# Kernel optimization log

Hardware: AMD Instinct MI355X
Metric: run time of the kernel (lower is better)

Reference implementation:

```python
import jax, jax.numpy as jnp
import numpy as np

L = 11
THETA_DIV = 5
OMEGA0 = 6
BLUR_K = 7
BLUR_SIGMA = 4.0


def _make_psi(j_scale):
    # Morlet wavelet bank exactly as np.fromfunction in the torch module
    c = L // 2
    k = np.arange(THETA_DIV, dtype=np.float64)[:, None, None]
    i = np.arange(L, dtype=np.float64)[None, :, None]
    jj = np.arange(L, dtype=np.float64)[None, None, :]
    scale = 2.0 * 2.0 ** (2 * j_scale)
    arg = (1j * OMEGA0 * ((i - c) * np.cos(np.pi * k / THETA_DIV)
                          - (jj - c) * np.sin(np.pi * k / THETA_DIV)) / scale
           - ((i - c) ** 2 + (jj - c) ** 2) / scale)
    return (1.0 / (np.sqrt(2.0 * np.pi) * 2.0 ** j_scale)) * np.exp(arg)


def _make_blur_kernel():
    # 7x7 Gaussian, sigma=4, normalized to sum 1 (standard GaussianBlur)
    c = (BLUR_K - 1) / 2.0
    x = np.arange(BLUR_K, dtype=np.float64) - c
    g = np.exp(-(x ** 2) / (2.0 * BLUR_SIGMA ** 2))
    k2 = np.outer(g, g)
    return (k2 / k2.sum()).astype(np.float32)


def setup_inputs() -> dict:
    key = jax.random.key(0)
    img = jax.random.normal(key, (8, 1, 256, 256), dtype=jnp.float32)
    psi = np.concatenate([_make_psi(3), _make_psi(0)], axis=0)  # [10,11,11] complex
    psi_re = jnp.asarray(psi.real.astype(np.float32)[:, None, :, :])  # [10,1,11,11]
    psi_im = jnp.asarray(psi.imag.astype(np.float32)[:, None, :, :])
    blur_k = jnp.asarray(_make_blur_kernel())  # [7,7]
    return {"img": img, "psi_re": psi_re, "psi_im": psi_im, "blur_k": blur_k}


def _conv(x, w, groups=1, pad=5):
    return jax.lax.conv_general_dilated(
        x, w, window_strides=(1, 1), padding=[(pad, pad), (pad, pad)],
        dimension_numbers=("NCHW", "OIHW", "NCHW"), feature_group_count=groups)


def _blur(x, blur_k):
    # depthwise Gaussian blur, padding 'same'
    C = x.shape[1]
    w = jnp.tile(blur_k[None, None], (C, 1, 1, 1))  # [C,1,7,7]
    return _conv(x, w, groups=C, pad=BLUR_K // 2)


def reference(img, psi_re, psi_im, blur_k):
    # s0: blurred input, strided downsample by 8
    s0 = _blur(img, blur_k)[:, :, ::8, ::8]

    # s1 = conv2d(img_complex, psi1): img is real, so split into re/im real convs
    s1_re = _conv(img, psi_re)            # [N,10,H,W]
    s1_im = _conv(img, psi_im)
    s1_abs = jnp.sqrt(s1_re * s1_re + s1_im * s1_im)
    # blurred s1 is later cast to double -> only its real part survives;
    # blur is a real-linear op so Re(blur(s1)) = blur(Re(s1))
    s1_out = _blur(s1_re, blur_k)[:, :, ::8, ::8]

    # s2 = grouped conv of |s1| with psi2 (psi1 tiled over 10 groups)
    psi2_re = jnp.tile(psi_re, (10, 1, 1, 1))  # [100,1,11,11]
    # only real part of blur(s2) reaches the output (cast to double)
    s2_re = _conv(s1_abs, psi2_re, groups=10)  # [N,100,H,W]
    s2_out = _blur(s2_re, blur_k)[:, :, ::8, ::8]

    feature = jnp.concatenate([s0, s1_out, s2_out], axis=1)  # [N,111,H/8,W/8]
    N = feature.shape[0]
    return feature.reshape(N, -1)
```

## Files before the change

kernel.cpp:

```cpp
#include <hip/hip_runtime.h>
#include <math.h>


#define PIMG_SZ (288 * 288)
#define FHP_OFF (8 * PIMG_SZ)
#define SSTR  284
#define W1    298
#define S1SZ  (17 * 298)
#define IVSTR 300
#define IVPL  (17 * 300)
#define CSTR  600

__global__ __launch_bounds__(256) void k_prep(const float* __restrict__ img,
                                              const float* __restrict__ psi_re,
                                              const float* __restrict__ psi_im,
                                              const float* __restrict__ blur,
                                              float* __restrict__ pimg,
                                              float* __restrict__ fhp) {
    int bid = blockIdx.x, tid = threadIdx.x;
    if (bid < 288) {
        int n = bid / 36, rg = bid - n * 36;
        float* dst = pimg + n * PIMG_SZ + rg * 8 * 288;
        const float* src = img + n * 65536;
        for (int i = tid; i < 576; i += 256) {
            int lr = i / 72, c4 = i - lr * 72;
            int prow = rg * 8 + lr;
            int irow = prow - 16;
            float4 v = {0.f, 0.f, 0.f, 0.f};
            if (irow >= 0 && irow < 256 && c4 >= 4 && c4 < 68)
                v = *(const float4*)(src + irow * 256 + 4 * c4 - 16);
            *(float4*)(dst + lr * 288 + 4 * c4) = v;
        }
        return;
    }
    for (int g = tid; g < 1360; g += 256) {
        int ch = g / 136;
        int w = g - ch * 136;
        int part = w / 17;
        int i = w - part * 17;
        const float* pr = psi_re + ch * 121;
        const float* pi = psi_im + ch * 121;
        float val = 0.f;
        if (part < 4) {
            int qmin = (part >= 2) ? 3 : 0;
            int comp = part & 1;
            float bden = blur[24];
            for (int q = qmin; q < 7; ++q) {
                int jj = i - q;
                if (jj < 0 || jj > 10) continue;
                float bq = blur[21 + q] / bden;
                float hh = comp ? pi[55 + jj] : pr[55 + jj];
                val += bq * hh;
            }
        } else {
            int pmin = (part >= 6) ? 3 : 0;
            int comp = part & 1;
            float dr = pr[60], di = pi[60];
            float inv = 1.f / (dr * dr + di * di);
            for (int p = pmin; p < 7; ++p) {
                int ii = i - p;
                if (ii < 0 || ii > 10) continue;
                float ap = blur[p * 7 + 3];
                float nr = pr[ii * 11 + 5], ni = pi[ii * 11 + 5];
                float f = comp ? (ni * dr - nr * di) * inv
                               : (nr * dr + ni * di) * inv;
                val += ap * f;
            }
        }
        fhp[g] = val;
    }
}

__global__ __launch_bounds__(512, 4) void k_fused4(const float* __restrict__ pimg,
                                                   const float* __restrict__ psi_re,
                                                   const float* __restrict__ psi_im,
                                                   const float* __restrict__ blur,
                                                   const float* __restrict__ fhp,
                                                   float* __restrict__ out) {
    __shared__ __align__(16) float bufA[10132];
    __shared__ __align__(16) float bufB[10200];
    const int tid = threadIdx.x;
    const int lane = tid & 63;
    const int wave = tid >> 6;
    const int Y = blockIdx.x;
    const int src2 = blockIdx.y;
    const int n = blockIdx.z;
    size_t nb = (size_t)n * 111 * 1024;

    const bool isimg = (src2 == 0);
    const bool paired = (src2 >= 3);
    int ga = 0, gb = 0;
    if (src2 == 1) ga = gb = 0;
    else if (src2 == 2) ga = gb = 5;
    else if (paired) {
        int p2 = src2 - 3;
        ga = (p2 < 2) ? 1 + p2 : 4 + p2;
        gb = (p2 < 2) ? 4 - p2 : 11 - p2;
    }

    if (isimg) {
        const float* gp = pimg + n * PIMG_SZ + (8 * Y + 8) * 288 + 8;
        for (int idx = tid; idx < 17 * 68; idx += 512) {
            int r = idx / 68, c4 = idx - r * 68;
            float4 v = *(const float4*)(gp + r * 288 + 4 * c4);
            int c = 4 * c4;
            int d = r * W1 + c + (c >> 3);
            bufA[d] = v.x; bufA[d + 1] = v.y; bufA[d + 2] = v.z; bufA[d + 3] = v.w;
        }
    } else {
        const float* pr = psi_re + ga * 121;
        const float* pi = psi_im + ga * 121;
        float dr = pr[60], di = pi[60];
        float inv = rsqrtf(dr * dr + di * di);

        const float* gp = pimg + n * PIMG_SZ + (8 * Y + 3) * 288 + 8;
        for (int idx = tid; idx < 27 * 68; idx += 512) {
            int r = idx / 68, c4 = idx - r * 68;
            *(float4*)(bufA + r * SSTR + 4 * c4) = *(const float4*)(gp + r * 288 + 4 * c4);
        }
        __syncthreads();

        for (int task = tid; task < 532; task += 512) {
            int rg = (task >= 266) ? 1 : 0;
            int v = task - rg * 266;
            int r0 = rg * 8;
            const float* sp = bufA + r0 * SSTR + v + 3;
            float xv[18];
#pragma unroll
            for (int p = 0; p < 18; ++p) xv[p] = sp[p * SSTR];
            int dsw = v + (v >> 3);
            float* dR = bufB + r0 * IVSTR + dsw;
#pragma unroll
            for (int m = 0; m < 8; ++m) {
                float ar = 0.f, ai = 0.f;
#pragma unroll
                for (int p = 0; p < 11; ++p) {
                    ar = fmaf(pr[p * 11 + 5], xv[m + p], ar);
                    ai = fmaf(pi[p * 11 + 5], xv[m + p], ai);
                }
                dR[m * IVSTR] = ar;
                dR[m * IVSTR + IVPL] = ai;
            }
        }
        if (tid < 266) {
            int v = tid;
            const float* sp = bufA + 16 * SSTR + v + 3;
            float ar = 0.f, ai = 0.f;
#pragma unroll
            for (int p = 0; p < 11; ++p) {
                float x = sp[p * SSTR];
                ar = fmaf(pr[p * 11 + 5], x, ar);
                ai = fmaf(pi[p * 11 + 5], x, ai);
            }
            int dsw = v + (v >> 3);
            bufB[16 * IVSTR + dsw] = ar;
            bufB[16 * IVSTR + IVPL + dsw] = ai;
        }
        __syncthreads();

        int rowbase = 8 * Y - 8;
        for (int t2 = tid; t2 < 544; t2 += 512) {
            int r = t2 >> 5, xg = t2 & 31;
            int ry = rowbase + r;
            int wb = r * W1 + 9 * xg + 9;
            if (ry >= 0 && ry < 256) {
                const float* sR = bufB + r * IVSTR + 9 * xg;
                float xr[18], xi[18];
#pragma unroll
                for (int j = 0; j < 18; ++j) {
                    int off = j + (j >> 3);
                    xr[j] = sR[off];
                    xi[j] = sR[off + IVPL];
                }
                if (paired) {
#pragma unroll
                    for (int m = 0; m < 8; ++m) {
                        float a = 0.f, b = 0.f, c = 0.f, d = 0.f;
#pragma unroll
                        for (int j = 0; j < 11; ++j) {
                            float hr = pr[55 + j], hi2 = pi[55 + j];
                            a = fmaf(hr, xr[m + j], a);
                            b = fmaf(hi2, xi[m + j], b);
                            c = fmaf(hr, xi[m + j], c);
                            d = fmaf(hi2, xr[m + j], d);
                        }
                        float e1 = a - b, o1 = c + d;
                        float e2 = a + b, o2 = c - d;
                        bufA[wb + m]        = inv * sqrtf(fmaf(e1, e1, o1 * o1));
                        bufA[S1SZ + wb + m] = inv * sqrtf(fmaf(e2, e2, o2 * o2));
                    }
                } else {
#pragma unroll
                    for (int m = 0; m < 8; ++m) {
                        float sr = 0.f, si = 0.f;
#pragma unroll
                        for (int j = 0; j < 11; ++j) {
                            float hr = pr[55 + j], hi2 = pi[55 + j];
                            sr = fmaf(hr, xr[m + j], fmaf(-hi2, xi[m + j], sr));
                            si = fmaf(hr, xi[m + j], fmaf(hi2, xr[m + j], si));
                        }
                        bufA[wb + m] = inv * sqrtf(fmaf(sr, sr, si * si));
                    }
                }
            } else {
#pragma unroll
                for (int m = 0; m < 8; ++m) {
                    bufA[wb + m] = 0.f;
                    if (paired) bufA[S1SZ + wb + m] = 0.f;
                }
            }
        }
        if (tid < 17) {
            int r = tid;
#pragma unroll
            for (int t = 0; t < 8; ++t) {
                bufA[r * W1 + t] = 0.f;
                if (paired) bufA[S1SZ + r * W1 + t] = 0.f;
            }
            bufA[r * W1 + 297] = 0.f;
            if (paired) bufA[S1SZ + r * W1 + 297] = 0.f;
        }
    }
    __syncthreads();

    {
        int kh = __builtin_amdgcn_readfirstlane(wave >> 2);
        int fro = (Y == 0) ? 102 : 68;
        int fio = (Y == 0) ? 119 : 85;
        const float* s1base = bufA + (paired ? kh * S1SZ : 0);
        auto doC = [&](int t) {
            int tsw = t + (t >> 3);
            float v[17];
#pragma unroll
            for (int i = 0; i < 17; ++i) v[i] = s1base[i * W1 + tsw];
            int nk = paired ? 6 : 3;
            for (int kk = 0; kk < nk; ++kk) {
                int k, p;
                if (paired) { k = (kk < 3) ? kk : kk + 2; p = kh * 6 + kk; }
                else        { k = kh * 5 + kk;            p = kh * 3 + kk; }
                const float* fR = fhp + k * 136 + fro;
                const float* fI = fhp + k * 136 + fio;
                float cr = 0.f, ci = 0.f;
#pragma unroll
                for (int i = 0; i < 17; ++i) {
                    cr = fmaf(fR[i], v[i], cr);
                    ci = fmaf(fI[i], v[i], ci);
                }
                bufB[p * CSTR + tsw] = cr;
                bufB[p * CSTR + 300 + tsw] = ci;
            }
        };
        doC(((wave & 3) << 6) + lane);
        if (lane < 9 && (wave == 0 || wave == 4))
            doC(256 + lane);
    }
    __syncthreads();

    int nout = paired ? 384 : 192;
    if (tid < nout) {
        int chsel = paired ? (tid >= 192) : 0;
        int t3 = tid - chsel * 192;
        int s = t3 >> 5, X = t3 & 31;
        int kdist = (s < 3) ? s : s + 2;
        int p = chsel * 6 + s;
        const float* hb = fhp + kdist * 136 + ((X == 0) ? 34 : 0);
        const float* cR = bufB + p * CSTR + 9 * X;
        float u = 0.f, v2 = 0.f;
#pragma unroll
        for (int j = 0; j < 17; ++j) {
            int off = j + (j >> 3);
            u  = fmaf(hb[j], cR[off], u);
            v2 = fmaf(hb[17 + j], cR[off + 300], v2);
        }
        int g = chsel ? gb : ga;
        int ch0 = isimg ? 1 : 11 + g * 10;
        out[nb + (size_t)(ch0 + kdist) * 1024 + Y * 32 + X] = u - v2;
        if (s == 1 || s == 2 || s == 4 || s == 5) {
            int partner = (s < 3) ? 5 - s : 13 - s;
            out[nb + (size_t)(ch0 + partner) * 1024 + Y * 32 + X] = u + v2;
        }
    } else if (isimg && tid < 224) {
        int X = tid - 192;
        float s0 = 0.f;
#pragma unroll
        for (int p = 0; p < 7; ++p)
#pragma unroll
            for (int q = 0; q < 7; ++q) {
                int c = 8 * X + q + 5;
                s0 = fmaf(blur[p * 7 + q], bufA[(p + 5) * W1 + c + (c >> 3)], s0);
            }
        out[nb + Y * 32 + X] = s0;
    }
}

extern "C" void kernel_launch(void* const* d_in, const int* in_sizes, int n_in,
                              void* d_out, int out_size, void* d_ws, size_t ws_size,
                              hipStream_t stream) {
    const float* img    = (const float*)d_in[0];
    const float* psi_re = (const float*)d_in[1];
    const float* psi_im = (const float*)d_in[2];
    const float* blur   = (const float*)d_in[3];
    float* out = (float*)d_out;
    float* ws = (float*)d_ws;
    float* pimg = ws;
    float* fhp  = ws + FHP_OFF;

    k_prep<<<289, 256, 0, stream>>>(img, psi_re, psi_im, blur, pimg, fhp);

    dim3 g2(32, 7, 8);
    k_fused4<<<g2, 512, 0, stream>>>(pimg, psi_re, psi_im, blur, fhp, out);
}
```

Baseline: 61.26 us.

## Split fused kernel into image and paired-group kernels with unrolled accumulators

The single multi-role kernel is split into two kernels. A dedicated image kernel handles the input-blur and first-order outputs with a smaller shared-memory footprint. A specialized paired kernel treats every wavelet group, including the two self-paired groups 0 and 5, through the paired path, so the role branches disappear. The column-filter stage is rewritten to read each shared value once and update six (or three) real/imag accumulator pairs in a fully unrolled loop. In exchange, the self-paired groups now do duplicate paired work and write their outputs from both halves, and there is an extra kernel launch.

```diff
diff --git a/kernel.cpp b/kernel.cpp
--- a/kernel.cpp
+++ b/kernel.cpp
@@ -71,155 +71,201 @@
     }
 }
 
-__global__ __launch_bounds__(512, 4) void k_fused4(const float* __restrict__ pimg,
-                                                   const float* __restrict__ psi_re,
-                                                   const float* __restrict__ psi_im,
-                                                   const float* __restrict__ blur,
-                                                   const float* __restrict__ fhp,
-                                                   float* __restrict__ out) {
+__global__ __launch_bounds__(512, 2) void k_img(const float* __restrict__ pimg,
+                                                const float* __restrict__ blur,
+                                                const float* __restrict__ fhp,
+                                                float* __restrict__ out) {
+    __shared__ __align__(16) float bufA[5080];
+    __shared__ __align__(16) float bufB[3600];
+    const int tid = threadIdx.x;
+    const int lane = tid & 63;
+    const int wave = tid >> 6;
+    const int Y = blockIdx.x;
+    const int n = blockIdx.z;
+    size_t nb = (size_t)n * 111 * 1024;
+
+    const float* gp = pimg + n * PIMG_SZ + (8 * Y + 8) * 288 + 8;
+    for (int idx = tid; idx < 17 * 68; idx += 512) {
+        int r = idx / 68, c4 = idx - r * 68;
+        float4 v = *(const float4*)(gp + r * 288 + 4 * c4);
+        int c = 4 * c4;
+        int d = r * W1 + c + (c >> 3);
+        bufA[d] = v.x; bufA[d + 1] = v.y; bufA[d + 2] = v.z; bufA[d + 3] = v.w;
+    }
+    __syncthreads();
+
+    {
+        int kh = __builtin_amdgcn_readfirstlane(wave >> 2);
+        int fro = (Y == 0) ? 102 : 68;
+        int fio = (Y == 0) ? 119 : 85;
+        const float* fb = fhp + kh * 680;
+        auto doC = [&](int t) {
+            int tsw = t + (t >> 3);
+            float cr0 = 0.f, ci0 = 0.f, cr1 = 0.f, ci1 = 0.f, cr2 = 0.f, ci2 = 0.f;
+#pragma unroll
+            for (int i = 0; i < 17; ++i) {
+                float v = bufA[i * W1 + tsw];
+                cr0 = fmaf(fb[fro + i], v, cr0);        ci0 = fmaf(fb[fio + i], v, ci0);
+                cr1 = fmaf(fb[136 + fro + i], v, cr1);  ci1 = fmaf(fb[136 + fio + i], v, ci1);
+                cr2 = fmaf(fb[272 + fro + i], v, cr2);  ci2 = fmaf(fb[272 + fio + i], v, ci2);
+            }
+            int p = kh * 3;
+            bufB[p * CSTR + tsw] = cr0;       bufB[p * CSTR + 300 + tsw] = ci0;
+            bufB[(p + 1) * CSTR + tsw] = cr1; bufB[(p + 1) * CSTR + 300 + tsw] = ci1;
+            bufB[(p + 2) * CSTR + tsw] = cr2; bufB[(p + 2) * CSTR + 300 + tsw] = ci2;
+        };
+        doC(((wave & 3) << 6) + lane);
+        if (lane < 9 && (wave == 0 || wave == 4)) doC(256 + lane);
+    }
+    __syncthreads();
+
+    if (tid < 192) {
+        int s = tid >> 5, X = tid & 31;
+        int kdist = (s < 3) ? s : s + 2;
+        const float* hb = fhp + kdist * 136 + ((X == 0) ? 34 : 0);
+        const float* cR = bufB + s * CSTR + 9 * X;
+        float u = 0.f, v2 = 0.f;
+#pragma unroll
+        for (int j = 0; j < 17; ++j) {
+            int off = j + (j >> 3);
+            u  = fmaf(hb[j], cR[off], u);
+            v2 = fmaf(hb[17 + j], cR[off + 300], v2);
+        }
+        out[nb + (size_t)(1 + kdist) * 1024 + Y * 32 + X] = u - v2;
+        if (s == 1 || s == 2 || s == 4 || s == 5) {
+            int partner = (s < 3) ? 5 - s : 13 - s;
+            out[nb + (size_t)(1 + partner) * 1024 + Y * 32 + X] = u + v2;
+        }
+    } else if (tid < 224) {
+        int X = tid - 192;
+        float s0 = 0.f;
+#pragma unroll
+        for (int p = 0; p < 7; ++p)
+#pragma unroll
+            for (int q = 0; q < 7; ++q) {
+                int c = 8 * X + q + 5;
+                s0 = fmaf(blur[p * 7 + q], bufA[(p + 5) * W1 + c + (c >> 3)], s0);
+            }
+        out[nb + Y * 32 + X] = s0;
+    }
+}
+
+__global__ __launch_bounds__(512, 4) void k_pairk(const float* __restrict__ pimg,
+                                                  const float* __restrict__ psi_re,
+                                                  const float* __restrict__ psi_im,
+                                                  const float* __restrict__ fhp,
+                                                  float* __restrict__ out) {
     __shared__ __align__(16) float bufA[10132];
     __shared__ __align__(16) float bufB[10200];
     const int tid = threadIdx.x;
     const int lane = tid & 63;
     const int wave = tid >> 6;
     const int Y = blockIdx.x;
-    const int src2 = blockIdx.y;
+    const int pidx = blockIdx.y;
     const int n = blockIdx.z;
     size_t nb = (size_t)n * 111 * 1024;
 
-    const bool isimg = (src2 == 0);
-    const bool paired = (src2 >= 3);
-    int ga = 0, gb = 0;
-    if (src2 == 1) ga = gb = 0;
-    else if (src2 == 2) ga = gb = 5;
-    else if (paired) {
-        int p2 = src2 - 3;
-        ga = (p2 < 2) ? 1 + p2 : 4 + p2;
-        gb = (p2 < 2) ? 4 - p2 : 11 - p2;
-    }
-
-    if (isimg) {
-        const float* gp = pimg + n * PIMG_SZ + (8 * Y + 8) * 288 + 8;
-        for (int idx = tid; idx < 17 * 68; idx += 512) {
-            int r = idx / 68, c4 = idx - r * 68;
-            float4 v = *(const float4*)(gp + r * 288 + 4 * c4);
-            int c = 4 * c4;
-            int d = r * W1 + c + (c >> 3);
-            bufA[d] = v.x; bufA[d + 1] = v.y; bufA[d + 2] = v.z; bufA[d + 3] = v.w;
-        }
-    } else {
-        const float* pr = psi_re + ga * 121;
-        const float* pi = psi_im + ga * 121;
-        float dr = pr[60], di = pi[60];
-        float inv = rsqrtf(dr * dr + di * di);
-
-        const float* gp = pimg + n * PIMG_SZ + (8 * Y + 3) * 288 + 8;
-        for (int idx = tid; idx < 27 * 68; idx += 512) {
-            int r = idx / 68, c4 = idx - r * 68;
-            *(float4*)(bufA + r * SSTR + 4 * c4) = *(const float4*)(gp + r * 288 + 4 * c4);
-        }
-        __syncthreads();
-
-        for (int task = tid; task < 532; task += 512) {
-            int rg = (task >= 266) ? 1 : 0;
-            int v = task - rg * 266;
-            int r0 = rg * 8;
-            const float* sp = bufA + r0 * SSTR + v + 3;
-            float xv[18];
-#pragma unroll
-            for (int p = 0; p < 18; ++p) xv[p] = sp[p * SSTR];
-            int dsw = v + (v >> 3);
-            float* dR = bufB + r0 * IVSTR + dsw;
+    const int gtab_a[6] = {0, 5, 1, 2, 6, 7};
+    const int gtab_b[6] = {0, 5, 4, 3, 9, 8};
+    int ga = gtab_a[pidx], gb = gtab_b[pidx];
+
+    const float* pr = psi_re + ga * 121;
+    const float* pi = psi_im + ga * 121;
+    float dr = pr[60], di = pi[60];
+    float inv = rsqrtf(dr * dr + di * di);
+
+    const float* gp = pimg + n * PIMG_SZ + (8 * Y + 3) * 288 + 8;
+    for (int idx = tid; idx < 27 * 68; idx += 512) {
+        int r = idx / 68, c4 = idx - r * 68;
+        *(float4*)(bufA + r * SSTR + 4 * c4) = *(const float4*)(gp + r * 288 + 4 * c4);
+    }
+    __syncthreads();
+
+    for (int task = tid; task < 532; task += 512) {
+        int rg = (task >= 266) ? 1 : 0;
+        int v = task - rg * 266;
+        int r0 = rg * 8;
+        const float* sp = bufA + r0 * SSTR + v + 3;
+        float xv[18];
+#pragma unroll
+        for (int p = 0; p < 18; ++p) xv[p] = sp[p * SSTR];
+        int dsw = v + (v >> 3);
+        float* dR = bufB + r0 * IVSTR + dsw;
+#pragma unroll
+        for (int m = 0; m < 8; ++m) {
+            float ar = 0.f, ai = 0.f;
+#pragma unroll
+            for (int p = 0; p < 11; ++p) {
+                ar = fmaf(pr[p * 11 + 5], xv[m + p], ar);
+                ai = fmaf(pi[p * 11 + 5], xv[m + p], ai);
+            }
+            dR[m * IVSTR] = ar;
+            dR[m * IVSTR + IVPL] = ai;
+        }
+    }
+    if (tid < 266) {
+        int v = tid;
+        const float* sp = bufA + 16 * SSTR + v + 3;
+        float ar = 0.f, ai = 0.f;
+#pragma unroll
+        for (int p = 0; p < 11; ++p) {
+            float x = sp[p * SSTR];
+            ar = fmaf(pr[p * 11 + 5], x, ar);
+            ai = fmaf(pi[p * 11 + 5], x, ai);
+        }
+        int dsw = v + (v >> 3);
+        bufB[16 * IVSTR + dsw] = ar;
+        bufB[16 * IVSTR + IVPL + dsw] = ai;
+    }
+    __syncthreads();
+
+    int rowbase = 8 * Y - 8;
+    for (int t2 = tid; t2 < 544; t2 += 512) {
+        int r = t2 >> 5, xg = t2 & 31;
+        int ry = rowbase + r;
+        int wb = r * W1 + 9 * xg + 9;
+        if (ry >= 0 && ry < 256) {
+            const float* sR = bufB + r * IVSTR + 9 * xg;
+            float xr[18], xi[18];
+#pragma unroll
+            for (int j = 0; j < 18; ++j) {
+                int off = j + (j >> 3);
+                xr[j] = sR[off];
+                xi[j] = sR[off + IVPL];
+            }
 #pragma unroll
             for (int m = 0; m < 8; ++m) {
-                float ar = 0.f, ai = 0.f;
-#pragma unroll
-                for (int p = 0; p < 11; ++p) {
-                    ar = fmaf(pr[p * 11 + 5], xv[m + p], ar);
-                    ai = fmaf(pi[p * 11 + 5], xv[m + p], ai);
+                float a = 0.f, b = 0.f, c = 0.f, d = 0.f;
+#pragma unroll
+                for (int j = 0; j < 11; ++j) {
+                    float hr = pr[55 + j], hi2 = pi[55 + j];
+                    a = fmaf(hr, xr[m + j], a);
+                    b = fmaf(hi2, xi[m + j], b);
+                    c = fmaf(hr, xi[m + j], c);
+                    d = fmaf(hi2, xr[m + j], d);
                 }
-                dR[m * IVSTR] = ar;
-                dR[m * IVSTR + IVPL] = ai;
-            }
-        }
-        if (tid < 266) {
-            int v = tid;
-            const float* sp = bufA + 16 * SSTR + v + 3;
-            float ar = 0.f, ai = 0.f;
-#pragma unroll
-            for (int p = 0; p < 11; ++p) {
-                float x = sp[p * SSTR];
-                ar = fmaf(pr[p * 11 + 5], x, ar);
-                ai = fmaf(pi[p * 11 + 5], x, ai);
-            }
-            int dsw = v + (v >> 3);
-            bufB[16 * IVSTR + dsw] = ar;
-            bufB[16 * IVSTR + IVPL + dsw] = ai;
-        }
-        __syncthreads();
-
-        int rowbase = 8 * Y - 8;
-        for (int t2 = tid; t2 < 544; t2 += 512) {
-            int r = t2 >> 5, xg = t2 & 31;
-            int ry = rowbase + r;
-            int wb = r * W1 + 9 * xg + 9;
-            if (ry >= 0 && ry < 256) {
-                const float* sR = bufB + r * IVSTR + 9 * xg;
-                float xr[18], xi[18];
-#pragma unroll
-                for (int j = 0; j < 18; ++j) {
-                    int off = j + (j >> 3);
-                    xr[j] = sR[off];
-                    xi[j] = sR[off + IVPL];
-                }
-                if (paired) {
-#pragma unroll
-                    for (int m = 0; m < 8; ++m) {
-                        float a = 0.f, b = 0.f, c = 0.f, d = 0.f;
-#pragma unroll
-                        for (int j = 0; j < 11; ++j) {
-                            float hr = pr[55 + j], hi2 = pi[55 + j];
-                            a = fmaf(hr, xr[m + j], a);
-                            b = fmaf(hi2, xi[m + j], b);
-                            c = fmaf(hr, xi[m + j], c);
-                            d = fmaf(hi2, xr[m + j], d);
-                        }
-                        float e1 = a - b, o1 = c + d;
-                        float e2 = a + b, o2 = c - d;
-                        bufA[wb + m]        = inv * sqrtf(fmaf(e1, e1, o1 * o1));
-                        bufA[S1SZ + wb + m] = inv * sqrtf(fmaf(e2, e2, o2 * o2));
-                    }
-                } else {
-#pragma unroll
-                    for (int m = 0; m < 8; ++m) {
-                        float sr = 0.f, si = 0.f;
-#pragma unroll
-                        for (int j = 0; j < 11; ++j) {
-                            float hr = pr[55 + j], hi2 = pi[55 + j];
-                            sr = fmaf(hr, xr[m + j], fmaf(-hi2, xi[m + j], sr));
-                            si = fmaf(hr, xi[m + j], fmaf(hi2, xr[m + j], si));
-                        }
-                        bufA[wb + m] = inv * sqrtf(fmaf(sr, sr, si * si));
-                    }
-                }
-            } else {
-#pragma unroll
-                for (int m = 0; m < 8; ++m) {
-                    bufA[wb + m] = 0.f;
-                    if (paired) bufA[S1SZ + wb + m] = 0.f;
-                }
-            }
-        }
-        if (tid < 17) {
-            int r = tid;
-#pragma unroll
-            for (int t = 0; t < 8; ++t) {
-                bufA[r * W1 + t] = 0.f;
-                if (paired) bufA[S1SZ + r * W1 + t] = 0.f;
-            }
-            bufA[r * W1 + 297] = 0.f;
-            if (paired) bufA[S1SZ + r * W1 + 297] = 0.f;
-        }
+                float e1 = a - b, o1 = c + d;
+                float e2 = a + b, o2 = c - d;
+                bufA[wb + m]        = inv * sqrtf(fmaf(e1, e1, o1 * o1));
+                bufA[S1SZ + wb + m] = inv * sqrtf(fmaf(e2, e2, o2 * o2));
+            }
+        } else {
+#pragma unroll
+            for (int m = 0; m < 8; ++m) {
+                bufA[wb + m] = 0.f;
+                bufA[S1SZ + wb + m] = 0.f;
+            }
+        }
+    }
+    if (tid < 17) {
+        int r = tid;
+#pragma unroll
+        for (int t = 0; t < 8; ++t) {
+            bufA[r * W1 + t] = 0.f;
+            bufA[S1SZ + r * W1 + t] = 0.f;
+        }
+        bufA[r * W1 + 297] = 0.f;
+        bufA[S1SZ + r * W1 + 297] = 0.f;
     }
     __syncthreads();
 
@@ -227,38 +273,38 @@
         int kh = __builtin_amdgcn_readfirstlane(wave >> 2);
         int fro = (Y == 0) ? 102 : 68;
         int fio = (Y == 0) ? 119 : 85;
-        const float* s1base = bufA + (paired ? kh * S1SZ : 0);
+        const float* s1b = bufA + kh * S1SZ;
+        const float* f0 = fhp + 0 * 136, *f1 = fhp + 1 * 136, *f2 = fhp + 2 * 136;
+        const float* f5 = fhp + 5 * 136, *f6 = fhp + 6 * 136, *f7 = fhp + 7 * 136;
         auto doC = [&](int t) {
             int tsw = t + (t >> 3);
-            float v[17];
-#pragma unroll
-            for (int i = 0; i < 17; ++i) v[i] = s1base[i * W1 + tsw];
-            int nk = paired ? 6 : 3;
-            for (int kk = 0; kk < nk; ++kk) {
-                int k, p;
-                if (paired) { k = (kk < 3) ? kk : kk + 2; p = kh * 6 + kk; }
-                else        { k = kh * 5 + kk;            p = kh * 3 + kk; }
-                const float* fR = fhp + k * 136 + fro;
-                const float* fI = fhp + k * 136 + fio;
-                float cr = 0.f, ci = 0.f;
-#pragma unroll
-                for (int i = 0; i < 17; ++i) {
-                    cr = fmaf(fR[i], v[i], cr);
-                    ci = fmaf(fI[i], v[i], ci);
-                }
-                bufB[p * CSTR + tsw] = cr;
-                bufB[p * CSTR + 300 + tsw] = ci;
-            }
+            float cr0 = 0.f, ci0 = 0.f, cr1 = 0.f, ci1 = 0.f, cr2 = 0.f, ci2 = 0.f;
+            float cr3 = 0.f, ci3 = 0.f, cr4 = 0.f, ci4 = 0.f, cr5 = 0.f, ci5 = 0.f;
+#pragma unroll
+            for (int i = 0; i < 17; ++i) {
+                float v = s1b[i * W1 + tsw];
+                cr0 = fmaf(f0[fro + i], v, cr0); ci0 = fmaf(f0[fio + i], v, ci0);
+                cr1 = fmaf(f1[fro + i], v, cr1); ci1 = fmaf(f1[fio + i], v, ci1);
+                cr2 = fmaf(f2[fro + i], v, cr2); ci2 = fmaf(f2[fio + i], v, ci2);
+                cr3 = fmaf(f5[fro + i], v, cr3); ci3 = fmaf(f5[fio + i], v, ci3);
+                cr4 = fmaf(f6[fro + i], v, cr4); ci4 = fmaf(f6[fio + i], v, ci4);
+                cr5 = fmaf(f7[fro + i], v, cr5); ci5 = fmaf(f7[fio + i], v, ci5);
+            }
+            float* cb = bufB + kh * 6 * CSTR + tsw;
+            cb[0] = cr0;          cb[300] = ci0;
+            cb[CSTR] = cr1;       cb[CSTR + 300] = ci1;
+            cb[2 * CSTR] = cr2;   cb[2 * CSTR + 300] = ci2;
+            cb[3 * CSTR] = cr3;   cb[3 * CSTR + 300] = ci3;
+            cb[4 * CSTR] = cr4;   cb[4 * CSTR + 300] = ci4;
+            cb[5 * CSTR] = cr5;   cb[5 * CSTR + 300] = ci5;
         };
         doC(((wave & 3) << 6) + lane);
-        if (lane < 9 && (wave == 0 || wave == 4))
-            doC(256 + lane);
-    }
-    __syncthreads();
-
-    int nout = paired ? 384 : 192;
-    if (tid < nout) {
-        int chsel = paired ? (tid >= 192) : 0;
+        if (lane < 9 && (wave == 0 || wave == 4)) doC(256 + lane);
+    }
+    __syncthreads();
+
+    if (tid < 384) {
+        int chsel = (tid >= 192) ? 1 : 0;
         int t3 = tid - chsel * 192;
         int s = t3 >> 5, X = t3 & 31;
         int kdist = (s < 3) ? s : s + 2;
@@ -273,23 +319,12 @@
             v2 = fmaf(hb[17 + j], cR[off + 300], v2);
         }
         int g = chsel ? gb : ga;
-        int ch0 = isimg ? 1 : 11 + g * 10;
+        int ch0 = 11 + g * 10;
         out[nb + (size_t)(ch0 + kdist) * 1024 + Y * 32 + X] = u - v2;
         if (s == 1 || s == 2 || s == 4 || s == 5) {
             int partner = (s < 3) ? 5 - s : 13 - s;
             out[nb + (size_t)(ch0 + partner) * 1024 + Y * 32 + X] = u + v2;
         }
-    } else if (isimg && tid < 224) {
-        int X = tid - 192;
-        float s0 = 0.f;
-#pragma unroll
-        for (int p = 0; p < 7; ++p)
-#pragma unroll
-            for (int q = 0; q < 7; ++q) {
-                int c = 8 * X + q + 5;
-                s0 = fmaf(blur[p * 7 + q], bufA[(p + 5) * W1 + c + (c >> 3)], s0);
-            }
-        out[nb + Y * 32 + X] = s0;
     }
 }
 
@@ -307,6 +342,9 @@
 
     k_prep<<<289, 256, 0, stream>>>(img, psi_re, psi_im, blur, pimg, fhp);
 
-    dim3 g2(32, 7, 8);
-    k_fused4<<<g2, 512, 0, stream>>>(pimg, psi_re, psi_im, blur, fhp, out);
+    dim3 gi(32, 1, 8);
+    k_img<<<gi, 512, 0, stream>>>(pimg, blur, fhp, out);
+
+    dim3 gpair(32, 6, 8);
+    k_pairk<<<gpair, 512, 0, stream>>>(pimg, psi_re, psi_im, fhp, out);
 }
```

Result: slower. 131.9 us (+115.2%).
